# Performance work log

Measured on AMD Instinct MI355X. Metric: run time of the kernel, lower is better.

## Reference

```python
import math
import jax, jax.numpy as jnp
import numpy as np

# --- Cayley-Dickson octonion structure constants: e_i * e_j = sign * e_{i XOR j} ---
def _cd_tables(levels=3):
    idx = np.array([[0]]); sgn = np.array([[1]])
    for _ in range(levels):
        n = idx.shape[0]; N = 2 * n
        I = np.zeros((N, N), np.int64); S = np.zeros((N, N), np.int64)
        cj = lambda j: 1 if j == 0 else -1  # conj sign of basis element j
        for i in range(n):
            for j in range(n):
                I[i, j] = idx[i, j];             S[i, j] = sgn[i, j]
                I[i, n + j] = n + idx[j, i];     S[i, n + j] = sgn[j, i]
                I[n + i, j] = n + idx[i, j];     S[n + i, j] = sgn[i, j] * cj(j)
                I[n + i, n + j] = idx[j, i];     S[n + i, n + j] = -cj(j) * sgn[j, i]
        idx, sgn = I, S
    return idx, sgn

_OIDX, _OSGN = _cd_tables()
# Octonion-structured linear: out_i = sum_j SIGN[i,j] * x_j @ W[WIDX[i,j]], WIDX[i,j]=i^j
_WIDX = np.array([[i ^ j for j in range(8)] for i in range(8)], np.int64)
_SIGN = np.array([[_OSGN[j, i ^ j] for j in range(8)] for i in range(8)], np.float32)


def _oct_linear(x, W):
    # x: [B,T,C], W: [8, C/8, C/8]
    B, T, C = x.shape
    Cp = C // 8
    parts = x.reshape(B, T, 8, Cp)
    Weff = jnp.asarray(_SIGN)[:, :, None, None] * W[jnp.asarray(_WIDX)]  # [8,8,Cp,Cp]
    return jnp.einsum('btjp,ijpq->btiq', parts, Weff).reshape(B, T, C)


def _rope(x, cos, sin):
    # x: [B,T,H,D]; consecutive channel pairs form complex numbers
    B, T, H, D = x.shape
    xr = x.reshape(B, T, H, D // 2, 2)
    xe, xo = xr[..., 0], xr[..., 1]
    c = cos[None, :, None, :]
    s = sin[None, :, None, :]
    return jnp.stack([xe * c - xo * s, xe * s + xo * c], axis=-1).reshape(B, T, H, D)


def _forward(x, Wq, Wk, Wv, Wo, mixer_W, mixer_beta, freqs_cos, freqs_sin):
    B, T, C = x.shape
    H = 32; D = C // H
    q = _oct_linear(x, Wq).reshape(B, T, H, D)
    k = _oct_linear(x, Wk).reshape(B, T, H, D)
    v = _oct_linear(x, Wv).reshape(B, T, H, D)
    q = _rope(q, freqs_cos, freqs_sin)
    k = _rope(k, freqs_cos, freqs_sin)
    q = q.transpose(0, 2, 1, 3)  # [B,H,T,D]
    k = k.transpose(0, 2, 1, 3)
    v = v.transpose(0, 2, 1, 3)
    scores = jnp.einsum('bhqd,bhkd->bhqk', q, k) / jnp.sqrt(jnp.float32(D))
    mask = jnp.tril(jnp.ones((T, T), bool))
    scores = jnp.where(mask, scores, jnp.finfo(scores.dtype).min)
    y = jnp.einsum('bhqk,bhkd->bhqd', jax.nn.softmax(scores, axis=-1), v)  # [B,H,T,D]
    # octonion head mixing in groups of 8 heads
    G = H // 8
    yg = y.reshape(B, G, 8, T, D)
    Weff = jnp.asarray(_SIGN)[:, :, None, None] * mixer_W[jnp.asarray(_WIDX)]  # [8,8,D,D]
    mixed = jnp.einsum('bgjtd,ijde->bgite', yg, Weff) * mixer_beta
    y = mixed.reshape(B, H, T, D).transpose(0, 2, 1, 3).reshape(B, T, C)
    return _oct_linear(y, Wo)


def setup_inputs() -> dict:
    key = jax.random.key(0)
    ks = jax.random.split(key, 8)
    B, T, C, H = 1, 2048, 4096, 32
    D = C // H; Cp = C // 8
    x = jax.random.normal(ks[0], (B, T, C), jnp.float32)
    Wq = jax.random.normal(ks[1], (8, Cp, Cp), jnp.float32) * 0.02
    Wk = jax.random.normal(ks[2], (8, Cp, Cp), jnp.float32) * 0.02
    Wv = jax.random.normal(ks[3], (8, Cp, Cp), jnp.float32) * 0.02
    Wo = jax.random.normal(ks[4], (8, Cp, Cp), jnp.float32) * 0.02
    mixer_W = jax.random.normal(ks[5], (8, D, D), jnp.float32) * 0.02
    mixer_beta = jnp.ones((D,), jnp.float32) * np.float32(math.sqrt(3.0 / (2.0 * D)))
    half = D // 2
    inv = 1.0 / (10000.0 ** (np.arange(half) * 2.0 / D))
    ang = np.arange(T)[:, None] * inv[None, :]
    freqs_cos = jnp.asarray(np.cos(ang), jnp.float32)
    freqs_sin = jnp.asarray(np.sin(ang), jnp.float32)
    return dict(x=x, Wq=Wq, Wk=Wk, Wv=Wv, Wo=Wo, mixer_W=mixer_W,
                mixer_beta=mixer_beta, freqs_cos=freqs_cos, freqs_sin=freqs_sin)


def reference(x, Wq, Wk, Wv, Wo, mixer_W, mixer_beta, freqs_cos, freqs_sin):
    return _forward(x, Wq, Wk, Wv, Wo, mixer_W, mixer_beta, freqs_cos, freqs_sin)
```

## Files before the change

kernel.cpp:

```cpp
#include <hip/hip_runtime.h>

typedef float f32x4 __attribute__((ext_vector_type(4)));
typedef __bf16 bf16x8 __attribute__((ext_vector_type(8)));
typedef unsigned short u16;
typedef u16 u16x8 __attribute__((ext_vector_type(8)));

__constant__ float c_osgn[64] = {
  1, 1, 1, 1, 1, 1, 1, 1,
  1,-1, 1,-1, 1,-1,-1, 1,
  1,-1,-1, 1, 1, 1,-1,-1,
  1, 1,-1,-1, 1,-1, 1,-1,
  1,-1,-1,-1,-1, 1, 1, 1,
  1, 1,-1, 1,-1,-1,-1, 1,
  1, 1, 1,-1,-1, 1,-1,-1,
  1,-1, 1, 1,-1,-1, 1,-1
};

__device__ __forceinline__ u16 f2bf(float f) {
  union { float f; unsigned u; } v; v.f = f;
  unsigned u = v.u;
  return (u16)((u + 0x7fffu + ((u >> 16) & 1u)) >> 16);
}
__device__ __forceinline__ float bf2f(u16 h) {
  union { unsigned u; float f; } v; v.u = ((unsigned)h) << 16;
  return v.f;
}

typedef const __attribute__((address_space(1))) void* as1cv;
typedef __attribute__((address_space(3))) void* as3v;
__device__ __forceinline__ void load16_lds(const void* g, void* l) {
  __builtin_amdgcn_global_load_lds((as1cv)g, (as3v)l, 16, 0, 0);
}

__global__ void conv_f32_bf16_vec(const float* __restrict__ src, u16* __restrict__ dst) {
  int i = blockIdx.x * 256 + threadIdx.x;
  float4 v = ((const float4*)src)[i];
  ushort4 o; o.x = f2bf(v.x); o.y = f2bf(v.y); o.z = f2bf(v.z); o.w = f2bf(v.w);
  ((ushort4*)dst)[i] = o;
}

__global__ __launch_bounds__(256) void transpose_w4(
    const float* __restrict__ Wq, const float* __restrict__ Wk,
    const float* __restrict__ Wv, const float* __restrict__ Wo,
    u16* __restrict__ WtB, long wsz) {
  __shared__ float t[64][65];
  const int zw = blockIdx.z;
  const int wsel = zw >> 3, w = zw & 7;
  const float* W = (wsel == 0) ? Wq : (wsel == 1) ? Wk : (wsel == 2) ? Wv : Wo;
  u16* Wt = WtB + wsel * wsz;
  const int p0 = blockIdx.y * 64, q0 = blockIdx.x * 64;
  const float* src = W + ((long)w * 512 + p0) * 512 + q0;
  const int tid = threadIdx.x;
  const int r = tid >> 2, c0 = (tid & 3) * 16;
#pragma unroll
  for (int j = 0; j < 4; j++) {
    float4 v = *(const float4*)(src + (long)r * 512 + c0 + j * 4);
    t[r][c0 + j * 4 + 0] = v.x; t[r][c0 + j * 4 + 1] = v.y;
    t[r][c0 + j * 4 + 2] = v.z; t[r][c0 + j * 4 + 3] = v.w;
  }
  __syncthreads();
  u16* dst = Wt + ((long)w * 512 + q0) * 512 + p0;
#pragma unroll
  for (int j = 0; j < 2; j++) {
    u16x8 o;
#pragma unroll
    for (int k = 0; k < 8; k++) o[k] = f2bf(t[c0 + j * 8 + k][r]);
    *(u16x8*)(dst + (long)r * 512 + c0 + j * 8) = o;
  }
}

__global__ void transpose_wm(const float* __restrict__ W, const float* __restrict__ beta,
                             u16* __restrict__ Wt) {
  int idx = blockIdx.x * 256 + threadIdx.x;
  int w = idx >> 14, rem = idx & 16383;
  int e = rem >> 7, d = rem & 127;
  Wt[(w << 14) + (e << 7) + d] = f2bf(W[(w << 14) + (d << 7) + e] * beta[e]);
}

__global__ __launch_bounds__(256, 2) void oct_gemmQKV(
    const u16* __restrict__ A, const u16* __restrict__ WtB,
    u16* __restrict__ out0, u16* __restrict__ out1, u16* __restrict__ out2,
    const float* __restrict__ fc, const float* __restrict__ fs, long wsz)
{
  __shared__ u16 smem[32768];

  const int nwg = gridDim.x * gridDim.y;
  const int lin = blockIdx.y * gridDim.x + blockIdx.x;
  const int swz = (lin & 7) * (nwg >> 3) + (lin >> 3);
  const int bx = swz % gridDim.x, by = swz / gridDim.x;

  const int np = bx * 128;
  const int bi = np >> 9;
  const int nsub = np & 511;
  const int bm = by * 128;
  const int h = np >> 7;

  const int tid = threadIdx.x;
  const int lane = tid & 63, w = tid >> 6;
  const int l15 = lane & 15, lg = lane >> 4;
  const int wm = w >> 1, wn = w & 1;
  const int srow = lane >> 3;
  const int sgr  = (lane & 7) ^ srow;

  f32x4 acc[3][4][4];
#pragma unroll
  for (int z = 0; z < 3; z++)
#pragma unroll
    for (int a = 0; a < 4; a++)
#pragma unroll
      for (int b = 0; b < 4; b++) acc[z][a][b] = f32x4{0.f, 0.f, 0.f, 0.f};

  for (int t = 0; t < 64; ++t) {
    const int k0 = t << 6;
    const int bj = t >> 3;
    const int widx = bi ^ bj;
    const unsigned xm = (c_osgn[bj * 8 + widx] < 0.f) ? 0x80008000u : 0u;
    const long woff = (long)widx * 262144 + (k0 & 511);

#pragma unroll
    for (int i = 0; i < 4; i++) {
      const int r = (w * 4 + i) * 8;
      load16_lds(A + (long)(bm + r + srow) * 4096 + k0 + sgr * 8,
                 (void*)(smem + r * 64));
    }
#pragma unroll
    for (int z = 0; z < 3; z++) {
      const u16* Wsrc = WtB + (long)z * wsz + woff;
#pragma unroll
      for (int i = 0; i < 4; i++) {
        const int r = (w * 4 + i) * 8;
        load16_lds(Wsrc + (long)(nsub + r + srow) * 512 + sgr * 8,
                   (void*)(smem + 8192 * (1 + z) + r * 64));
      }
    }
    __syncthreads();

#pragma unroll
    for (int kk = 0; kk < 64; kk += 32) {
      const int gsw = (((kk >> 3) + lg) ^ (l15 & 7)) * 8;
      uint4 a4[4];
#pragma unroll
      for (int mt = 0; mt < 4; mt++)
        a4[mt] = *(const uint4*)(smem + (wm * 64 + mt * 16 + l15) * 64 + gsw);
      if (xm) {
#pragma unroll
        for (int mt = 0; mt < 4; mt++) {
          a4[mt].x ^= xm; a4[mt].y ^= xm; a4[mt].z ^= xm; a4[mt].w ^= xm;
        }
      }
#pragma unroll
      for (int z = 0; z < 3; z++) {
        bf16x8 bF[4];
#pragma unroll
        for (int nt = 0; nt < 4; nt++)
          bF[nt] = *(const bf16x8*)(smem + 8192 * (1 + z) +
                                    (wn * 64 + nt * 16 + l15) * 64 + gsw);
#pragma unroll
        for (int mt = 0; mt < 4; mt++)
#pragma unroll
          for (int nt = 0; nt < 4; nt++)
            acc[z][mt][nt] = __builtin_amdgcn_mfma_f32_16x16x32_bf16(
                *(const bf16x8*)&a4[mt], bF[nt], acc[z][mt][nt], 0, 0, 0);
      }
    }
    __syncthreads();
  }

#pragma unroll
  for (int z = 0; z < 2; z++) {
    u16* dq = (z == 0) ? out0 : out1;
#pragma unroll
    for (int mt = 0; mt < 4; mt++)
#pragma unroll
      for (int nt = 0; nt < 4; nt++) {
        const int d = wn * 64 + nt * 16 + l15;
        const int p = d >> 1;
        const bool ev = (l15 & 1) == 0;
#pragma unroll
        for (int j = 0; j < 4; j++) {
          const int trow = bm + wm * 64 + mt * 16 + 4 * lg + j;
          const float v = acc[z][mt][nt][j];
          const float sh = __shfl_xor(v, 1);
          const float c = fc[trow * 64 + p];
          const float s = fs[trow * 64 + p];
          const float o = ev ? (v * c - sh * s) : (sh * s + v * c);
          dq[((long)h * 2048 + trow) * 128 + d] = f2bf(o);
        }
      }
  }

#pragma unroll
  for (int dh = 0; dh < 2; ++dh) {
    __syncthreads();
    if (wn == dh) {
#pragma unroll
      for (int mt = 0; mt < 4; mt++)
#pragma unroll
        for (int nt = 0; nt < 4; nt++)
#pragma unroll
          for (int j = 0; j < 4; j++)
            smem[(nt * 16 + l15) * 152 + wm * 64 + mt * 16 + 4 * lg + j] =
                f2bf(acc[2][mt][nt][j]);
    }
    __syncthreads();
#pragma unroll
    for (int p = 0; p < 4; ++p) {
      const int dl = p * 16 + (tid >> 4);
      const int tt = (tid & 15) * 8;
      u16x8 o = *(const u16x8*)(smem + dl * 152 + tt);
      *(u16x8*)(out2 + ((long)h * 128 + dh * 64 + dl) * 2048 + bm + tt) = o;
    }
  }
}

template <int MODE>
__global__ __launch_bounds__(256, 3) void oct_gemm128(
    const u16* __restrict__ A, const u16* __restrict__ WtB,
    void* __restrict__ out0,
    int K, int lda, int ldo,
    int slab_shift, int bs_shift, long wslab, long oslab, long acolslab)
{
  __shared__ u16 smem[16384];
  const int NT = K >> 6;
  const int BS = 1 << bs_shift;
  const long wblk = (long)BS * BS;

  const int nwg = gridDim.x * gridDim.y;
  const int lin = blockIdx.y * gridDim.x + blockIdx.x;
  const int swz = (lin & 7) * (nwg >> 3) + (lin >> 3);
  const int bx = swz % gridDim.x, by = swz / gridDim.x;

  const int nglob = bx * 128;
  const int z = nglob >> slab_shift;
  const int np = nglob & ((1 << slab_shift) - 1);
  const int bi = np >> bs_shift;
  const int nsub = np & (BS - 1);
  const int bm = by * 128;
  const u16* Wt = WtB + (long)z * wslab;
  const long acol0 = (long)z * acolslab;

  const int tid = threadIdx.x;
  const int lane = tid & 63, w = tid >> 6;
  const int l15 = lane & 15, lg = lane >> 4;
  const int wm = w >> 1, wn = w & 1;
  const int srow = lane >> 3;
  const int sgr  = (lane & 7) ^ srow;

  f32x4 acc[4][4];
#pragma unroll
  for (int a = 0; a < 4; a++)
#pragma unroll
    for (int b = 0; b < 4; b++) acc[a][b] = f32x4{0.f, 0.f, 0.f, 0.f};

  for (int t = 0; t < NT; ++t) {
    const int k0 = t << 6;
    const int bj = k0 >> bs_shift;
    const int widx = bi ^ bj;
    const unsigned xm = (c_osgn[bj * 8 + widx] < 0.f) ? 0x80008000u : 0u;
    const u16* Wsrc = Wt + (long)widx * wblk + (k0 & (BS - 1));

#pragma unroll
    for (int i = 0; i < 4; i++) {
      const int r = (w * 4 + i) * 8;
      load16_lds(A + (long)(bm + r + srow) * lda + acol0 + k0 + sgr * 8,
                 (void*)(smem + r * 64));
    }
#pragma unroll
    for (int i = 0; i < 4; i++) {
      const int r = (w * 4 + i) * 8;
      load16_lds(Wsrc + (long)(nsub + r + srow) * BS + sgr * 8,
                 (void*)(smem + 8192 + r * 64));
    }
    __syncthreads();

#pragma unroll
    for (int kk = 0; kk < 64; kk += 32) {
      const int gsw = (((kk >> 3) + lg) ^ (l15 & 7)) * 8;
      uint4 a4[4];
      bf16x8 bF[4];
#pragma unroll
      for (int mt = 0; mt < 4; mt++)
        a4[mt] = *(const uint4*)(smem + (wm * 64 + mt * 16 + l15) * 64 + gsw);
      if (xm) {
#pragma unroll
        for (int mt = 0; mt < 4; mt++) {
          a4[mt].x ^= xm; a4[mt].y ^= xm; a4[mt].z ^= xm; a4[mt].w ^= xm;
        }
      }
#pragma unroll
      for (int nt = 0; nt < 4; nt++)
        bF[nt] = *(const bf16x8*)(smem + 8192 + (wn * 64 + nt * 16 + l15) * 64 + gsw);
#pragma unroll
      for (int mt = 0; mt < 4; mt++)
#pragma unroll
        for (int nt = 0; nt < 4; nt++)
          acc[mt][nt] = __builtin_amdgcn_mfma_f32_16x16x32_bf16(
              *(const bf16x8*)&a4[mt], bF[nt], acc[mt][nt], 0, 0, 0);
    }
    __syncthreads();
  }

#pragma unroll
  for (int mt = 0; mt < 4; mt++)
#pragma unroll
    for (int nt = 0; nt < 4; nt++)
#pragma unroll
      for (int j = 0; j < 4; j++) {
        const int row = bm + wm * 64 + mt * 16 + 4 * lg + j;
        const int col = np + wn * 64 + nt * 16 + l15;
        const float v = acc[mt][nt][j];
        if constexpr (MODE == 0)
          ((u16*)out0)[(long)z * oslab + (long)row * ldo + col] = f2bf(v);
        else
          ((float*)out0)[(long)row * ldo + col] = v;
      }
}

__global__ __launch_bounds__(256, 2) void attn5(
    const u16* __restrict__ qR, const u16* __restrict__ kR,
    const u16* __restrict__ vT, u16* __restrict__ y)
{
  const int bid = blockIdx.x;
  const int h = bid & 31;
  const int qb = 31 - (bid >> 5);
  const int q0 = qb * 64;

  const int tid = threadIdx.x;
  const int lane = tid & 63, w = tid >> 6;
  const int l15 = lane & 15, lg = lane >> 4;

  __shared__ u16 Ks[2][64][128];
  __shared__ u16 Vs[2][128][64];
  __shared__ u16 Ps[4][16][64];

  auto stageK = [&](int kb, int buf) {
    const long kbase = (long)h * 2048 + (long)kb * 64;
#pragma unroll
    for (int i = 0; i < 4; i++) {
      const int j = w * 4 + i;
      const int row = j * 4 + (lane >> 4);
      const int sg = (lane & 15) ^ (row & 7);
      load16_lds(kR + (kbase + row) * 128 + sg * 8, (void*)&Ks[buf][j * 4][0]);
    }
  };
  auto stageV = [&](int kb, int buf) {
    const long vbase = (long)h * 128 * 2048 + (long)kb * 64;
#pragma unroll
    for (int i = 0; i < 4; i++) {
      const int j = w * 4 + i;
      const int row = j * 8 + (lane >> 3);
      const int sg = (lane & 7) ^ (row & 7);
      load16_lds(vT + vbase + (long)row * 2048 + sg * 8, (void*)&Vs[buf][j * 8][0]);
    }
  };

  stageK(0, 0);
  stageV(0, 0);

  bf16x8 aQ[4];
  {
    const long qbase = ((long)h * 2048 + q0 + w * 16 + l15) * 128;
#pragma unroll
    for (int c = 0; c < 4; c++)
      aQ[c] = *(const bf16x8*)(qR + qbase + 32 * c + 8 * lg);
  }

  bf16x8 ones;
#pragma unroll
  for (int j = 0; j < 8; j++) ones[j] = (__bf16)1.0f;

  f32x4 Y[8], LS;
#pragma unroll
  for (int dt = 0; dt < 8; dt++) Y[dt] = f32x4{0.f, 0.f, 0.f, 0.f};
  LS = f32x4{0.f, 0.f, 0.f, 0.f};

  const float scale = 0.08838834764831845f;
  const int nkb = qb + 1;

  for (int kb = 0; kb < nkb; kb++) {
    const int buf = kb & 1;
    const int k0 = kb * 64;
    if (kb + 1 < nkb) { stageK(kb + 1, buf ^ 1); stageV(kb + 1, buf ^ 1); }
    if (kb + 1 < nkb) asm volatile("s_waitcnt vmcnt(8)" ::: "memory");
    else              asm volatile("s_waitcnt vmcnt(0)" ::: "memory");
    __builtin_amdgcn_s_barrier();
    asm volatile("" ::: "memory");

    f32x4 S[4];
#pragma unroll
    for (int ks = 0; ks < 4; ks++) S[ks] = f32x4{0.f, 0.f, 0.f, 0.f};
#pragma unroll
    for (int c = 0; c < 4; c++) {
      bf16x8 bK[4];
#pragma unroll
      for (int ks = 0; ks < 4; ks++)
        bK[ks] = *(const bf16x8*)&Ks[buf][ks * 16 + l15][(((4 * c + lg) ^ (l15 & 7)) * 8)];
#pragma unroll
      for (int ks = 0; ks < 4; ks++)
        S[ks] = __builtin_amdgcn_mfma_f32_16x16x32_bf16(aQ[c], bK[ks], S[ks], 0, 0, 0);
    }

    {
      const int qrow0 = q0 + w * 16 + 4 * lg;
#pragma unroll
      for (int ks = 0; ks < 4; ks++) {
        const int kg = k0 + ks * 16 + l15;
#pragma unroll
        for (int rr = 0; rr < 4; rr++) {
          const float e = __expf(fmaf(S[ks][rr], scale, -32.f));
          S[ks][rr] = (kg > qrow0 + rr) ? 0.f : e;
        }
      }
#pragma unroll
      for (int ks = 0; ks < 4; ks++)
#pragma unroll
        for (int rr = 0; rr < 4; rr++) {
          const int row = 4 * lg + rr;
          const int G = (2 * ks + (l15 >> 3)) ^ (row & 7);
          Ps[w][row][G * 8 + (l15 & 7)] = f2bf(S[ks][rr]);
        }
    }

#pragma unroll
    for (int kk = 0; kk < 2; kk++) {
      const int pg = ((4 * kk + lg) ^ (l15 & 7)) * 8;
      bf16x8 pF = *(const bf16x8*)&Ps[w][l15][pg];
#pragma unroll
      for (int dt = 0; dt < 8; dt++) {
        bf16x8 vF = *(const bf16x8*)&Vs[buf][dt * 16 + l15][pg];
        Y[dt] = __builtin_amdgcn_mfma_f32_16x16x32_bf16(pF, vF, Y[dt], 0, 0, 0);
      }
      LS = __builtin_amdgcn_mfma_f32_16x16x32_bf16(pF, ones, LS, 0, 0, 0);
    }
    asm volatile("" ::: "memory");
    __builtin_amdgcn_s_barrier();
    asm volatile("" ::: "memory");
  }

  float inv[4];
#pragma unroll
  for (int rr = 0; rr < 4; rr++) inv[rr] = 1.0f / LS[rr];
#pragma unroll
  for (int dt = 0; dt < 8; dt++)
#pragma unroll
    for (int rr = 0; rr < 4; rr++)
      y[(long)(q0 + w * 16 + 4 * lg + rr) * 4096 + h * 128 + dt * 16 + l15] =
          f2bf(Y[dt][rr] * inv[rr]);
}

extern "C" void kernel_launch(void* const* d_in, const int* in_sizes, int n_in,
                              void* d_out, int out_size, void* d_ws, size_t ws_size,
                              hipStream_t stream) {
  const float* x    = (const float*)d_in[0];
  const float* Wq   = (const float*)d_in[1];
  const float* Wk   = (const float*)d_in[2];
  const float* Wv   = (const float*)d_in[3];
  const float* Wo   = (const float*)d_in[4];
  const float* Wm   = (const float*)d_in[5];
  const float* beta = (const float*)d_in[6];
  const float* fc   = (const float*)d_in[7];
  const float* fs   = (const float*)d_in[8];
  float* out = (float*)d_out;

  const long TC = 2048L * 4096L;
  const long WSZ = 8L * 512 * 512;
  u16* ws  = (u16*)d_ws;
  u16* xb  = ws;
  u16* wt  = ws + TC;
  u16* wmt = wt + 4 * WSZ;
  u16* g3  = wmt + 131072L;
  u16* r3  = g3 + 3 * TC;
  u16* yatt = xb;
  u16* ymix = g3;

  conv_f32_bf16_vec<<<TC / 4 / 256, 256, 0, stream>>>(x, xb);
  transpose_w4<<<dim3(8, 8, 32), 256, 0, stream>>>(Wq, Wk, Wv, Wo, wt, WSZ);
  transpose_wm<<<512, 256, 0, stream>>>(Wm, beta, wmt);

  oct_gemmQKV<<<dim3(32, 16), 256, 0, stream>>>(
      xb, wt, r3, r3 + TC, r3 + 2 * TC, fc, fs, WSZ);

  attn5<<<1024, 256, 0, stream>>>(r3, r3 + TC, r3 + 2 * TC, yatt);

  oct_gemm128<0><<<dim3(32, 16), 256, 0, stream>>>(
      yatt, wmt, (void*)ymix,
      1024, 4096, 4096, 10, 7, 0L, 1024L, 1024L);

  oct_gemm128<2><<<dim3(32, 16), 256, 0, stream>>>(
      ymix, wt + 3 * WSZ, (void*)out,
      4096, 4096, 4096, 12, 9, 0L, 0L, 0L);
}
```

Measured before the change: 398.0 us.

## Double-buffer QKV GEMM loads and halve N tile to double grid

The fused QKV projection kernel now prefetches the next two K-steps of A and weight tiles into a double-buffered LDS region and uses vmcnt waits with raw barriers, so global loads overlap with MFMA work. The N tile per block shrinks from 128 to 64 columns and the grid doubles to 1024 blocks, which also shrinks the accumulator register footprint. The V-transpose epilogue is simplified to a single LDS pass. In exchange, the A tile is reloaded twice as often across blocks and more LDS is used per block, which may limit occupancy.

```diff
diff --git a/kernel.cpp b/kernel.cpp
--- a/kernel.cpp
+++ b/kernel.cpp
@@ -77,23 +77,24 @@
   Wt[(w << 14) + (e << 7) + d] = f2bf(W[(w << 14) + (d << 7) + e] * beta[e]);
 }
 
-__global__ __launch_bounds__(256, 2) void oct_gemmQKV(
+__global__ __launch_bounds__(256, 2) void oct_gemmQKV2(
     const u16* __restrict__ A, const u16* __restrict__ WtB,
     u16* __restrict__ out0, u16* __restrict__ out1, u16* __restrict__ out2,
     const float* __restrict__ fc, const float* __restrict__ fs, long wsz)
 {
-  __shared__ u16 smem[32768];
+  __shared__ u16 smem[40960];
 
   const int nwg = gridDim.x * gridDim.y;
   const int lin = blockIdx.y * gridDim.x + blockIdx.x;
   const int swz = (lin & 7) * (nwg >> 3) + (lin >> 3);
   const int bx = swz % gridDim.x, by = swz / gridDim.x;
 
-  const int np = bx * 128;
+  const int np = bx * 64;
   const int bi = np >> 9;
   const int nsub = np & 511;
   const int bm = by * 128;
   const int h = np >> 7;
+  const int dbase = np & 64;
 
   const int tid = threadIdx.x;
   const int lane = tid & 63, w = tid >> 6;
@@ -102,46 +103,57 @@
   const int srow = lane >> 3;
   const int sgr  = (lane & 7) ^ srow;
 
-  f32x4 acc[3][4][4];
+  f32x4 acc[3][4][2];
 #pragma unroll
   for (int z = 0; z < 3; z++)
 #pragma unroll
     for (int a = 0; a < 4; a++)
 #pragma unroll
-      for (int b = 0; b < 4; b++) acc[z][a][b] = f32x4{0.f, 0.f, 0.f, 0.f};
-
-  for (int t = 0; t < 64; ++t) {
+      for (int b = 0; b < 2; b++) acc[z][a][b] = f32x4{0.f, 0.f, 0.f, 0.f};
+
+  auto stage = [&](int t, int buf) {
     const int k0 = t << 6;
     const int bj = t >> 3;
     const int widx = bi ^ bj;
-    const unsigned xm = (c_osgn[bj * 8 + widx] < 0.f) ? 0x80008000u : 0u;
     const long woff = (long)widx * 262144 + (k0 & 511);
-
 #pragma unroll
     for (int i = 0; i < 4; i++) {
       const int r = (w * 4 + i) * 8;
       load16_lds(A + (long)(bm + r + srow) * 4096 + k0 + sgr * 8,
-                 (void*)(smem + r * 64));
+                 (void*)(smem + buf * 8192 + r * 64));
     }
 #pragma unroll
     for (int z = 0; z < 3; z++) {
       const u16* Wsrc = WtB + (long)z * wsz + woff;
 #pragma unroll
-      for (int i = 0; i < 4; i++) {
-        const int r = (w * 4 + i) * 8;
+      for (int i = 0; i < 2; i++) {
+        const int r = (w * 2 + i) * 8;
         load16_lds(Wsrc + (long)(nsub + r + srow) * 512 + sgr * 8,
-                   (void*)(smem + 8192 * (1 + z) + r * 64));
-      }
-    }
-    __syncthreads();
-
-#pragma unroll
-    for (int kk = 0; kk < 64; kk += 32) {
-      const int gsw = (((kk >> 3) + lg) ^ (l15 & 7)) * 8;
+                   (void*)(smem + 16384 + buf * 12288 + z * 4096 + r * 64));
+      }
+    }
+  };
+
+  stage(0, 0);
+  stage(1, 1);
+
+  for (int t = 0; t < 64; ++t) {
+    if (t + 1 < 64) asm volatile("s_waitcnt vmcnt(10)" ::: "memory");
+    else            asm volatile("s_waitcnt vmcnt(0)" ::: "memory");
+    __builtin_amdgcn_s_barrier();
+    asm volatile("" ::: "memory");
+
+    const int buf = t & 1;
+    const int bj = t >> 3;
+    const unsigned xm = (c_osgn[bj * 8 + (bi ^ bj)] < 0.f) ? 0x80008000u : 0u;
+
+#pragma unroll
+    for (int kk = 0; kk < 2; kk++) {
+      const int gsw = (((4 * kk) + lg) ^ (l15 & 7)) * 8;
       uint4 a4[4];
 #pragma unroll
       for (int mt = 0; mt < 4; mt++)
-        a4[mt] = *(const uint4*)(smem + (wm * 64 + mt * 16 + l15) * 64 + gsw);
+        a4[mt] = *(const uint4*)(smem + buf * 8192 + (wm * 64 + mt * 16 + l15) * 64 + gsw);
       if (xm) {
 #pragma unroll
         for (int mt = 0; mt < 4; mt++) {
@@ -150,20 +162,24 @@
       }
 #pragma unroll
       for (int z = 0; z < 3; z++) {
-        bf16x8 bF[4];
-#pragma unroll
-        for (int nt = 0; nt < 4; nt++)
-          bF[nt] = *(const bf16x8*)(smem + 8192 * (1 + z) +
-                                    (wn * 64 + nt * 16 + l15) * 64 + gsw);
+        bf16x8 bF[2];
+#pragma unroll
+        for (int nt = 0; nt < 2; nt++)
+          bF[nt] = *(const bf16x8*)(smem + 16384 + buf * 12288 + z * 4096 +
+                                    (wn * 32 + nt * 16 + l15) * 64 + gsw);
 #pragma unroll
         for (int mt = 0; mt < 4; mt++)
 #pragma unroll
-          for (int nt = 0; nt < 4; nt++)
+          for (int nt = 0; nt < 2; nt++)
             acc[z][mt][nt] = __builtin_amdgcn_mfma_f32_16x16x32_bf16(
                 *(const bf16x8*)&a4[mt], bF[nt], acc[z][mt][nt], 0, 0, 0);
       }
     }
-    __syncthreads();
+
+    asm volatile("" ::: "memory");
+    __builtin_amdgcn_s_barrier();
+    asm volatile("" ::: "memory");
+    if (t + 2 < 64) stage(t + 2, buf);
   }
 
 #pragma unroll
@@ -172,8 +188,8 @@
 #pragma unroll
     for (int mt = 0; mt < 4; mt++)
 #pragma unroll
-      for (int nt = 0; nt < 4; nt++) {
-        const int d = wn * 64 + nt * 16 + l15;
+      for (int nt = 0; nt < 2; nt++) {
+        const int d = dbase + wn * 32 + nt * 16 + l15;
         const int p = d >> 1;
         const bool ev = (l15 & 1) == 0;
 #pragma unroll
@@ -190,25 +206,21 @@
   }
 
 #pragma unroll
-  for (int dh = 0; dh < 2; ++dh) {
-    __syncthreads();
-    if (wn == dh) {
-#pragma unroll
-      for (int mt = 0; mt < 4; mt++)
-#pragma unroll
-        for (int nt = 0; nt < 4; nt++)
-#pragma unroll
-          for (int j = 0; j < 4; j++)
-            smem[(nt * 16 + l15) * 152 + wm * 64 + mt * 16 + 4 * lg + j] =
-                f2bf(acc[2][mt][nt][j]);
-    }
-    __syncthreads();
-#pragma unroll
-    for (int p = 0; p < 4; ++p) {
-      const int dl = p * 16 + (tid >> 4);
-      const int tt = (tid & 15) * 8;
-      u16x8 o = *(const u16x8*)(smem + dl * 152 + tt);
-      *(u16x8*)(out2 + ((long)h * 128 + dh * 64 + dl) * 2048 + bm + tt) = o;
+  for (int mt = 0; mt < 4; mt++)
+#pragma unroll
+    for (int nt = 0; nt < 2; nt++)
+#pragma unroll
+      for (int j = 0; j < 4; j++)
+        smem[(wn * 32 + nt * 16 + l15) * 136 + wm * 64 + mt * 16 + 4 * lg + j] =
+            f2bf(acc[2][mt][nt][j]);
+  __syncthreads();
+  {
+    const int dl = tid >> 2;
+    const int tc = (tid & 3) * 32;
+#pragma unroll
+    for (int q = 0; q < 4; q++) {
+      u16x8 o = *(const u16x8*)(smem + dl * 136 + tc + q * 8);
+      *(u16x8*)(out2 + ((long)h * 128 + dbase + dl) * 2048 + bm + tc + q * 8) = o;
     }
   }
 }
@@ -477,7 +489,7 @@
   transpose_w4<<<dim3(8, 8, 32), 256, 0, stream>>>(Wq, Wk, Wv, Wo, wt, WSZ);
   transpose_wm<<<512, 256, 0, stream>>>(Wm, beta, wmt);
 
-  oct_gemmQKV<<<dim3(32, 16), 256, 0, stream>>>(
+  oct_gemmQKV2<<<dim3(64, 16), 256, 0, stream>>>(
       xb, wt, r3, r3 + TC, r3 + 2 * TC, fc, fs, WSZ);
 
   attn5<<<1024, 256, 0, stream>>>(r3, r3 + TC, r3 + 2 * TC, yatt);
```

After: 415.2 us. 1.04x slower.
